# Optimization experiments

Measured on AMD Instinct MI355X. Metric: run time of the kernel, lower is better.

## Reference

```python
import jax, jax.numpy as jnp
import numpy as np

NEW_INDEX = jnp.array([7, 0, 1, 6, 8, 2, 5, 4, 3], dtype=jnp.int32)
B, S, D, PF, LF, A = 65536, 20000, 300, 12, 8, 8
IN_DIM = PF + LF + 1  # 21
NCHW = ('NCHW', 'OIHW', 'NCHW')


def setup_inputs() -> dict:
    key = jax.random.key(0)
    ks = jax.random.split(key, 18)
    state = jax.random.randint(ks[0], (B,), 0, S)
    des = jax.random.randint(ks[1], (B,), 0, D)
    act = jax.random.randint(ks[2], (B,), 0, A)
    action_state_pad = jnp.concatenate(
        [jax.random.randint(ks[3], (S, A), 0, S), jnp.arange(S)[:, None]], axis=1)
    policy_mask_pad = jnp.concatenate(
        [jax.random.randint(ks[4], (S, A), 0, 2), jnp.zeros((S, 1), jnp.int32)], axis=1)
    path_feature = jax.random.normal(ks[5], (S, D, PF), jnp.float32)
    link_feature = jax.random.normal(ks[6], (S, LF), jnp.float32)
    w = lambda k, shp: jax.random.normal(k, shp, jnp.float32) * 0.05
    return {
        'state': state, 'des': des, 'act': act,
        'action_state_pad': action_state_pad, 'policy_mask_pad': policy_mask_pad,
        'path_feature': path_feature, 'link_feature': link_feature,
        'conv1_w': w(ks[7], (20, IN_DIM, 3, 3)), 'conv1_b': w(ks[8], (20,)),
        'conv2_w': w(ks[9], (30, 20, 2, 2)), 'conv2_b': w(ks[10], (30,)),
        'fc1_w': w(ks[11], (120, 30 + A)), 'fc1_b': w(ks[12], (120,)),
        'fc2_w': w(ks[13], (84, 120)), 'fc2_b': w(ks[14], (84,)),
        'fc3_w': w(ks[15], (1, 84)), 'fc3_b': w(ks[16], (1,)),
    }


def _process_features(state, des, action_state_pad, policy_mask_pad, path_feature, link_feature):
    neigh = action_state_pad[state]                       # [B, 9]
    npf = path_feature[neigh, des[:, None], :]            # [B, 9, PF]
    nef = link_feature[neigh]                             # [B, 9, LF]
    nmf = policy_mask_pad[state][..., None].astype(npf.dtype)  # [B, 9, 1]
    feat = jnp.concatenate([npf, nef, nmf], axis=-1)[:, NEW_INDEX, :]  # [B, 9, 21]
    x = feat.reshape(feat.shape[0], 3, 3, -1)             # [B, 3, 3, 21]
    return x.transpose(0, 3, 1, 2)                        # [B, 21, 3, 3]


def reference(state, des, act, action_state_pad, policy_mask_pad, path_feature,
              link_feature, conv1_w, conv1_b, conv2_w, conv2_b,
              fc1_w, fc1_b, fc2_w, fc2_b, fc3_w, fc3_b):
    lrelu = lambda v: jax.nn.leaky_relu(v, 0.2)
    x = _process_features(state, des, action_state_pad, policy_mask_pad,
                          path_feature, link_feature)
    x = jax.lax.conv_general_dilated(x, conv1_w, (1, 1), ((1, 1), (1, 1)),
                                     dimension_numbers=NCHW) + conv1_b[:, None, None]
    x = lrelu(x)                                          # [B, 20, 3, 3]
    x = jax.lax.reduce_window(x, -jnp.inf, jax.lax.max,
                              (1, 1, 2, 2), (1, 1, 1, 1), 'VALID')  # [B, 20, 2, 2]
    x = jax.lax.conv_general_dilated(x, conv2_w, (1, 1), 'VALID',
                                     dimension_numbers=NCHW) + conv2_b[:, None, None]
    x = lrelu(x).reshape(-1, 30)                          # [B, 30]
    x = jnp.concatenate([x, jax.nn.one_hot(act, A, dtype=x.dtype)], axis=1)  # [B, 38]
    x = lrelu(x @ fc1_w.T + fc1_b)
    x = lrelu(x @ fc2_w.T + fc2_b)
    return jax.nn.sigmoid(x @ fc3_w.T + fc3_b)            # [B, 1]
```

## Files before the change

kernel.cpp:

```cpp
#include <hip/hip_runtime.h>
#include <hip/hip_bf16.h>
#include <math.h>

#define DDIM   300
#define PFN    12
#define LFN    8
#define ICH    21
#define TPB    256
#define SPB    64
#define SLOT_DW 99
#define W1N    3780
#define W2N    2400
#define FW1H   2280
#define FW2H   5040
#define BIASN  339
#define OB1    0
#define OB2    20
#define OFB1   50
#define OFB2   170
#define OFW3   254
#define OFB3   338

__device__ __forceinline__ float lrelu(float v) { return v > 0.0f ? v : 0.2f * v; }

__device__ __forceinline__ unsigned int pack2(float a, float b) {
    union { __hip_bfloat162 h; unsigned int u; } cv;
    cv.h.x = __float2bfloat16(a);
    cv.h.y = __float2bfloat16(b);
    return cv.u;
}
__device__ __forceinline__ float bflo(unsigned int u) {
    union { unsigned int i; float f; } c; c.i = u << 16; return c.f;
}
__device__ __forceinline__ float bfhi(unsigned int u) {
    union { unsigned int i; float f; } c; c.i = u & 0xffff0000u; return c.f;
}

__device__ __forceinline__ void conv_acc(float o[9], const float* __restrict__ w, const float fv[9]) {
#pragma unroll
    for (int t = 0; t < 9; ++t) {
        const int ky = t / 3 - 1, kx = t % 3 - 1;
        const float wv = w[t];
#pragma unroll
        for (int y = 0; y < 3; ++y) {
            const int iy = y + ky;
            if (iy < 0 || iy > 2) continue;
#pragma unroll
            for (int x = 0; x < 3; ++x) {
                const int ix = x + kx;
                if (ix < 0 || ix > 2) continue;
                o[y * 3 + x] = fmaf(wv, fv[iy * 3 + ix], o[y * 3 + x]);
            }
        }
    }
}

__launch_bounds__(TPB, 2)
__global__ void disc_kernel(
    const int* __restrict__ state, const int* __restrict__ des,
    const int* __restrict__ act,
    const int* __restrict__ asp_g,
    const int* __restrict__ pmp_g,
    const float* __restrict__ path_feature,
    const float* __restrict__ link_feature,
    const float* __restrict__ w1, const float* __restrict__ b1,
    const float* __restrict__ w2, const float* __restrict__ b2,
    const float* __restrict__ fw1, const float* __restrict__ fb1,
    const float* __restrict__ fw2, const float* __restrict__ fb2,
    const float* __restrict__ fw3, const float* __restrict__ fb3,
    float* __restrict__ out, int n)
{
    __shared__ __align__(16) float w1s[W1N];
    __shared__ __align__(16) float w2s[W2N];
    __shared__ __align__(16) unsigned int fw1h[FW1H];
    __shared__ __align__(16) unsigned int fw2h[FW2H];
    __shared__ float bias[BIASN];
    __shared__ unsigned int feat[SPB * SLOT_DW];

    const int tid = threadIdx.x;

    {
        const float4* s1 = (const float4*)w1;  float4* d1 = (float4*)w1s;
        for (int i = tid; i < W1N / 4; i += TPB) d1[i] = s1[i];
        const float4* s2 = (const float4*)w2;  float4* d2 = (float4*)w2s;
        for (int i = tid; i < W2N / 4; i += TPB) d2[i] = s2[i];
        const float2* sf1 = (const float2*)fw1;
        for (int i = tid; i < FW1H; i += TPB) { const float2 v = sf1[i]; fw1h[i] = pack2(v.x, v.y); }
        const float2* sf2 = (const float2*)fw2;
        for (int i = tid; i < FW2H; i += TPB) { const float2 v = sf2[i]; fw2h[i] = pack2(v.x, v.y); }
        for (int i = tid; i < BIASN; i += TPB) {
            float v;
            if      (i < OB2)  v = b1[i];
            else if (i < OFB1) v = b2[i - OB2];
            else if (i < OFB2) v = fb1[i - OFB1];
            else if (i < OFW3) v = fb2[i - OFB2];
            else if (i < OFB3) v = fw3[i - OFW3];
            else               v = fb3[0];
            bias[i] = v;
        }
    }
    __syncthreads();

    const int lane4  = tid & 3;
    const int lsamp  = tid >> 2;
    const int sample = blockIdx.x * SPB + lsamp;
    if (sample >= n) return;

    const int s  = state[sample];
    const int d  = des[sample];
    const int ai = act[sample];

    const int* asp = asp_g + s * 9;
    const int* pmp = pmp_g + s * 9;
    unsigned int* fslot = feat + lsamp * SLOT_DW;

#pragma unroll
    for (int t = 0; t < 3; ++t) {
        const int p = lane4 + 4 * t;
        if (p < 9) {
            const int a  = (int)((0x345286107ULL >> (4 * p)) & 0xF);
            const int na = asp[a];
            const float m = (float)pmp[a];
            const float4* pf = (const float4*)(path_feature + (na * DDIM + d) * PFN);
            const float4 v0 = pf[0], v1 = pf[1], v2 = pf[2];
            const float4* lf = (const float4*)(link_feature + na * LFN);
            const float4 u0 = lf[0], u1 = lf[1];
            unsigned int* dst = fslot + p * 11;
            dst[0] = pack2(v0.x, v0.y); dst[1] = pack2(v0.z, v0.w);
            dst[2] = pack2(v1.x, v1.y); dst[3] = pack2(v1.z, v1.w);
            dst[4] = pack2(v2.x, v2.y); dst[5] = pack2(v2.z, v2.w);
            dst[6] = pack2(u0.x, u0.y); dst[7] = pack2(u0.z, u0.w);
            dst[8] = pack2(u1.x, u1.y); dst[9] = pack2(u1.z, u1.w);
            dst[10] = pack2(m, 0.0f);
        }
    }
    asm volatile("s_waitcnt lgkmcnt(0)" ::: "memory");

    const int oc0 = lane4 * 5;
    float o[5][9];
#pragma unroll
    for (int c = 0; c < 5; ++c) {
        const float bb = bias[OB1 + oc0 + c];
#pragma unroll
        for (int q = 0; q < 9; ++q) o[c][q] = bb;
    }

#pragma unroll 1
    for (int icp = 0; icp < 10; ++icp) {
        unsigned int fw[9];
#pragma unroll
        for (int q = 0; q < 9; ++q) fw[q] = fslot[q * 11 + icp];
        float fv[9];
#pragma unroll
        for (int q = 0; q < 9; ++q) fv[q] = bflo(fw[q]);
#pragma unroll
        for (int c = 0; c < 5; ++c)
            conv_acc(o[c], w1s + ((oc0 + c) * ICH + 2 * icp) * 9, fv);
#pragma unroll
        for (int q = 0; q < 9; ++q) fv[q] = bfhi(fw[q]);
#pragma unroll
        for (int c = 0; c < 5; ++c)
            conv_acc(o[c], w1s + ((oc0 + c) * ICH + 2 * icp + 1) * 9, fv);
    }
    {
        float f20[9];
#pragma unroll
        for (int q = 0; q < 9; ++q) f20[q] = bflo(fslot[q * 11 + 10]);
#pragma unroll
        for (int c = 0; c < 5; ++c)
            conv_acc(o[c], w1s + ((oc0 + c) * ICH + 20) * 9, f20);
    }

    float pooled[5][4];
#pragma unroll
    for (int c = 0; c < 5; ++c) {
        float v[9];
#pragma unroll
        for (int q = 0; q < 9; ++q) v[q] = lrelu(o[c][q]);
        pooled[c][0] = fmaxf(fmaxf(v[0], v[1]), fmaxf(v[3], v[4]));
        pooled[c][1] = fmaxf(fmaxf(v[1], v[2]), fmaxf(v[4], v[5]));
        pooled[c][2] = fmaxf(fmaxf(v[3], v[4]), fmaxf(v[6], v[7]));
        pooled[c][3] = fmaxf(fmaxf(v[4], v[5]), fmaxf(v[7], v[8]));
    }

    float x30[30];
#pragma unroll
    for (int j = 0; j < 30; ++j) {
        const float4* wr = (const float4*)(w2s + j * 80 + oc0 * 4);
        float acc = 0.0f;
#pragma unroll
        for (int c = 0; c < 5; ++c) {
            const float4 wv = wr[c];
            acc = fmaf(wv.x, pooled[c][0], acc);
            acc = fmaf(wv.y, pooled[c][1], acc);
            acc = fmaf(wv.z, pooled[c][2], acc);
            acc = fmaf(wv.w, pooled[c][3], acc);
        }
        acc += __shfl_xor(acc, 1, 64);
        acc += __shfl_xor(acc, 2, 64);
        x30[j] = lrelu(acc + bias[OB2 + j]);
    }

    float h1[30];
    const int j0 = lane4 * 30;
    const int ohd  = (30 + ai) >> 1;
    const int ohodd = (30 + ai) & 1;
#pragma unroll
    for (int jj = 0; jj < 30; ++jj) {
        const unsigned int* wr = fw1h + (j0 + jj) * 19;
        const unsigned int uoh = wr[ohd];
        float acc = bias[OFB1 + j0 + jj] + (ohodd ? bfhi(uoh) : bflo(uoh));
#pragma unroll
        for (int m = 0; m < 15; ++m) {
            const unsigned int u = wr[m];
            acc = fmaf(bflo(u), x30[2 * m],     acc);
            acc = fmaf(bfhi(u), x30[2 * m + 1], acc);
        }
        h1[jj] = lrelu(acc);
    }

    float z = bias[OFB3];
#pragma unroll 2
    for (int i = 0; i < 84; ++i) {
        const unsigned int* wp = fw2h + i * 60 + lane4 * 15;
        float a = 0.0f;
#pragma unroll
        for (int m = 0; m < 15; ++m) {
            const unsigned int u = wp[m];
            a = fmaf(bflo(u), h1[2 * m],     a);
            a = fmaf(bfhi(u), h1[2 * m + 1], a);
        }
        a += __shfl_xor(a, 1, 64);
        a += __shfl_xor(a, 2, 64);
        z = fmaf(bias[OFW3 + i], lrelu(a + bias[OFB2 + i]), z);
    }

    if (lane4 == 0)
        out[sample] = 1.0f / (1.0f + __expf(-z));
}

extern "C" void kernel_launch(void* const* d_in, const int* in_sizes, int n_in,
                              void* d_out, int out_size, void* d_ws, size_t ws_size,
                              hipStream_t stream) {
    const int*   state = (const int*)d_in[0];
    const int*   des   = (const int*)d_in[1];
    const int*   act   = (const int*)d_in[2];
    const int*   asp   = (const int*)d_in[3];
    const int*   pmp   = (const int*)d_in[4];
    const float* pathf = (const float*)d_in[5];
    const float* linkf = (const float*)d_in[6];
    const float* w1    = (const float*)d_in[7];
    const float* b1    = (const float*)d_in[8];
    const float* w2    = (const float*)d_in[9];
    const float* b2    = (const float*)d_in[10];
    const float* fw1   = (const float*)d_in[11];
    const float* fb1   = (const float*)d_in[12];
    const float* fw2   = (const float*)d_in[13];
    const float* fb2   = (const float*)d_in[14];
    const float* fw3   = (const float*)d_in[15];
    const float* fb3   = (const float*)d_in[16];

    const int n = in_sizes[0];
    dim3 grid((n + SPB - 1) / SPB), block(TPB);
    hipLaunchKernelGGL(disc_kernel, grid, block, 0, stream,
                       state, des, act, asp, pmp, pathf, linkf,
                       w1, b1, w2, b2, fw1, fb1, fw2, fb2, fw3, fb3,
                       (float*)d_out, n);
}
```

Before: 512.2 us.

## Use v_dot2_f32_bf16 for conv1 and FC layers with bf16-packed weights

Conv1 weights are repacked into shared memory as bf16 pairs over adjacent input channels, and the convolution now uses the packed dot2 bf16 instruction on the paired feature words. This removes the separate unpack-and-FMA steps. fc1 and fc2 activations are packed to bf16 pairs so each inner product also uses dot2. This halves the FMA instruction count and shrinks the conv1 weight footprint in LDS. In exchange, conv1 weights and the intermediate activations are rounded to bf16, which lowers accuracy, and the weight staging now does scalar gathers with div/mod indexing.

Measured after the change: 459.9 us. 1.11x faster.

```diff
diff --git a/kernel.cpp b/kernel.cpp
--- a/kernel.cpp
+++ b/kernel.cpp
@@ -9,7 +9,7 @@
 #define TPB    256
 #define SPB    64
 #define SLOT_DW 99
-#define W1N    3780
+#define W1P    1980
 #define W2N    2400
 #define FW1H   2280
 #define FW2H   5040
@@ -36,11 +36,18 @@
     union { unsigned int i; float f; } c; c.i = u & 0xffff0000u; return c.f;
 }
 
-__device__ __forceinline__ void conv_acc(float o[9], const float* __restrict__ w, const float fv[9]) {
+__device__ __forceinline__ float dot2bf(unsigned int a, unsigned int b, float c) {
+    float d;
+    asm("v_dot2_f32_bf16 %0, %1, %2, %3" : "=v"(d) : "v"(a), "v"(b), "v"(c));
+    return d;
+}
+
+__device__ __forceinline__ void conv_acc2(float o[9], const unsigned int* __restrict__ w,
+                                          const unsigned int fv[9]) {
 #pragma unroll
     for (int t = 0; t < 9; ++t) {
         const int ky = t / 3 - 1, kx = t % 3 - 1;
-        const float wv = w[t];
+        const unsigned int wv = w[t];
 #pragma unroll
         for (int y = 0; y < 3; ++y) {
             const int iy = y + ky;
@@ -49,7 +56,7 @@
             for (int x = 0; x < 3; ++x) {
                 const int ix = x + kx;
                 if (ix < 0 || ix > 2) continue;
-                o[y * 3 + x] = fmaf(wv, fv[iy * 3 + ix], o[y * 3 + x]);
+                o[y * 3 + x] = dot2bf(wv, fv[iy * 3 + ix], o[y * 3 + x]);
             }
         }
     }
@@ -70,7 +77,7 @@
     const float* __restrict__ fw3, const float* __restrict__ fb3,
     float* __restrict__ out, int n)
 {
-    __shared__ __align__(16) float w1s[W1N];
+    __shared__ __align__(16) unsigned int w1p[W1P];
     __shared__ __align__(16) float w2s[W2N];
     __shared__ __align__(16) unsigned int fw1h[FW1H];
     __shared__ __align__(16) unsigned int fw2h[FW2H];
@@ -80,8 +87,12 @@
     const int tid = threadIdx.x;
 
     {
-        const float4* s1 = (const float4*)w1;  float4* d1 = (float4*)w1s;
-        for (int i = tid; i < W1N / 4; i += TPB) d1[i] = s1[i];
+        for (int i = tid; i < W1P; i += TPB) {
+            const int oc = i / 99, r = i % 99, icp = r / 9, t = r % 9;
+            const float lo = w1[(oc * ICH + 2 * icp) * 9 + t];
+            const float hi = (icp < 10) ? w1[(oc * ICH + 2 * icp + 1) * 9 + t] : 0.0f;
+            w1p[i] = pack2(lo, hi);
+        }
         const float4* s2 = (const float4*)w2;  float4* d2 = (float4*)w2s;
         for (int i = tid; i < W2N / 4; i += TPB) d2[i] = s2[i];
         const float2* sf1 = (const float2*)fw1;
@@ -146,29 +157,18 @@
     }
 
 #pragma unroll 1
-    for (int icp = 0; icp < 10; ++icp) {
-        unsigned int fw[9];
-#pragma unroll
-        for (int q = 0; q < 9; ++q) fw[q] = fslot[q * 11 + icp];
-        float fv[9];
-#pragma unroll
-        for (int q = 0; q < 9; ++q) fv[q] = bflo(fw[q]);
-#pragma unroll
-        for (int c = 0; c < 5; ++c)
-            conv_acc(o[c], w1s + ((oc0 + c) * ICH + 2 * icp) * 9, fv);
-#pragma unroll
-        for (int q = 0; q < 9; ++q) fv[q] = bfhi(fw[q]);
-#pragma unroll
-        for (int c = 0; c < 5; ++c)
-            conv_acc(o[c], w1s + ((oc0 + c) * ICH + 2 * icp + 1) * 9, fv);
-    }
-    {
-        float f20[9];
-#pragma unroll
-        for (int q = 0; q < 9; ++q) f20[q] = bflo(fslot[q * 11 + 10]);
-#pragma unroll
-        for (int c = 0; c < 5; ++c)
-            conv_acc(o[c], w1s + ((oc0 + c) * ICH + 20) * 9, f20);
+    for (int icp = 0; icp < 11; ++icp) {
+        unsigned int fwd[9];
+#pragma unroll
+        for (int q = 0; q < 9; ++q) fwd[q] = fslot[q * 11 + icp];
+        unsigned int wt[9];
+#pragma unroll
+        for (int c = 0; c < 5; ++c) {
+            const unsigned int* wrow = w1p + (oc0 + c) * 99 + icp * 9;
+#pragma unroll
+            for (int t = 0; t < 9; ++t) wt[t] = wrow[t];
+            conv_acc2(o[c], wt, fwd);
+        }
     }
 
     float pooled[5][4];
@@ -201,9 +201,13 @@
         x30[j] = lrelu(acc + bias[OB2 + j]);
     }
 
+    unsigned int xp[15];
+#pragma unroll
+    for (int m = 0; m < 15; ++m) xp[m] = pack2(x30[2 * m], x30[2 * m + 1]);
+
     float h1[30];
     const int j0 = lane4 * 30;
-    const int ohd  = (30 + ai) >> 1;
+    const int ohd   = (30 + ai) >> 1;
     const int ohodd = (30 + ai) & 1;
 #pragma unroll
     for (int jj = 0; jj < 30; ++jj) {
@@ -211,13 +215,14 @@
         const unsigned int uoh = wr[ohd];
         float acc = bias[OFB1 + j0 + jj] + (ohodd ? bfhi(uoh) : bflo(uoh));
 #pragma unroll
-        for (int m = 0; m < 15; ++m) {
-            const unsigned int u = wr[m];
-            acc = fmaf(bflo(u), x30[2 * m],     acc);
-            acc = fmaf(bfhi(u), x30[2 * m + 1], acc);
-        }
+        for (int m = 0; m < 15; ++m)
+            acc = dot2bf(wr[m], xp[m], acc);
         h1[jj] = lrelu(acc);
     }
+
+    unsigned int hp[15];
+#pragma unroll
+    for (int m = 0; m < 15; ++m) hp[m] = pack2(h1[2 * m], h1[2 * m + 1]);
 
     float z = bias[OFB3];
 #pragma unroll 2
@@ -225,11 +230,8 @@
         const unsigned int* wp = fw2h + i * 60 + lane4 * 15;
         float a = 0.0f;
 #pragma unroll
-        for (int m = 0; m < 15; ++m) {
-            const unsigned int u = wp[m];
-            a = fmaf(bflo(u), h1[2 * m],     a);
-            a = fmaf(bfhi(u), h1[2 * m + 1], a);
-        }
+        for (int m = 0; m < 15; ++m)
+            a = dot2bf(wp[m], hp[m], a);
         a += __shfl_xor(a, 1, 64);
         a += __shfl_xor(a, 2, 64);
         z = fmaf(bias[OFW3 + i], lrelu(a + bias[OFB2 + i]), z);
```
